# Kernel tuning notes

Measured on AMD Instinct MI355X. Metric: run time of the kernel, lower is better.

Reference implementation:

```python
import jax, jax.numpy as jnp
import numpy as np

N_NODES = 50000
N_EDGES = 800000
IN_NODE = 16
IN_EDGE = 8
HID = 128
N_LAYERS = 4
LN_EPS = 1e-5


def setup_inputs() -> dict:
    key = jax.random.key(0)
    ks = jax.random.split(key, 16)
    s = lambda k, shape, fan: jax.random.normal(k, shape, jnp.float32) * (1.0 / np.sqrt(fan))
    inp = {
        "x": jax.random.normal(ks[0], (N_NODES, IN_NODE), jnp.float32),
        "edge_index": jax.random.randint(ks[1], (2, N_EDGES), 0, N_NODES, jnp.int32),
        "edge_attr": jax.random.normal(ks[2], (N_EDGES, IN_EDGE), jnp.float32),
        # input projection
        "W_in": s(ks[3], (HID, IN_NODE), IN_NODE),
        "b_in": jnp.zeros((HID,), jnp.float32),
        # stacked SAGEConv params: lin_l (neighbors, biased), lin_r (root, no bias)
        "Wl": s(ks[4], (N_LAYERS, HID, HID), HID),
        "bl": jnp.zeros((N_LAYERS, HID), jnp.float32),
        "Wr": s(ks[5], (N_LAYERS, HID, HID), HID),
        # stacked LayerNorm params
        "ln_g": jnp.ones((N_LAYERS, HID), jnp.float32),
        "ln_b": jnp.zeros((N_LAYERS, HID), jnp.float32),
        # edge MLP: (2*HID+IN_EDGE) -> HID -> HID//2 -> 1
        "W1": s(ks[6], (HID, 2 * HID + IN_EDGE), 2 * HID + IN_EDGE),
        "b1": jnp.zeros((HID,), jnp.float32),
        "W2": s(ks[7], (HID // 2, HID), HID),
        "b2": jnp.zeros((HID // 2,), jnp.float32),
        "W3": s(ks[8], (1, HID // 2), HID // 2),
        "b3": jnp.zeros((1,), jnp.float32),
    }
    return inp


def reference(x, edge_index, edge_attr, W_in, b_in, Wl, bl, Wr, ln_g, ln_b, W1, b1, W2, b2, W3, b3):
    n = x.shape[0]
    src, dst = edge_index[0], edge_index[1]
    # in-degree for mean aggregation (clamped to 1, as in PyG mean aggr)
    deg = jax.ops.segment_sum(jnp.ones_like(dst, jnp.float32), dst, num_segments=n)
    deg = jnp.maximum(deg, 1.0)[:, None]  # [N,1]

    h = x @ W_in.T + b_in  # [N,H]

    def layer(h, params):
        Wl_i, bl_i, Wr_i, g_i, be_i = params
        # SAGEConv: mean of source features scattered to destinations
        agg = jax.ops.segment_sum(h[src], dst, num_segments=n) / deg
        h2 = agg @ Wl_i.T + bl_i + h @ Wr_i.T
        # LayerNorm
        mu = jnp.mean(h2, axis=-1, keepdims=True)
        var = jnp.mean(jnp.square(h2 - mu), axis=-1, keepdims=True)
        h2 = (h2 - mu) * jax.lax.rsqrt(var + LN_EPS) * g_i + be_i
        # ReLU (dropout = identity in eval mode)
        return jax.nn.relu(h2), None

    h, _ = jax.lax.scan(layer, h, (Wl, bl, Wr, ln_g, ln_b))

    # edge head: gather endpoints, concat with edge_attr, MLP -> scalar logit
    e = jnp.concatenate([h[src], h[dst], edge_attr], axis=1)  # [E, 2H+F_e]
    e = jax.nn.relu(e @ W1.T + b1)
    e = jax.nn.relu(e @ W2.T + b2)
    logits = (e @ W3.T + b3)[:, 0]  # [E]
    return logits
```

## Files before the change

### kernel.cpp

```cpp
#include <hip/hip_runtime.h>
#include <stdint.h>

#define NN 50000
#define NE 800000

#define O_WIN 0
#define O_BIN 2048
#define O_WL  2176
#define O_BL  67712
#define O_WR  68224
#define O_LNG 133760
#define O_LNB 134272
#define O_W1  134784
#define O_B1  168576
#define O_W2  168704
#define O_B2  176896
#define O_W3  176960
#define O_B3  177024
#define W_TOTAL 177025

#define WS_FLAGS 0
#define WS_WC    512
#define WS_CNT   355072
#define WS_ROWP  555520
#define WS_CUR   756224
#define WS_CSR   956928
#define WS_EID   4156928
#define WS_DST   7356928
#define WS_W1P   10556928
#define WS_HB0   10630656
#define WS_HB1   23430656
#define WS_NEED  36230656

#define SCAN_NB 196

#define HSTR 304
#define ASTR 560

typedef float f32x4 __attribute__((ext_vector_type(4)));
typedef short bf16x8 __attribute__((ext_vector_type(8)));
typedef short bf16x4 __attribute__((ext_vector_type(4)));

__device__ __forceinline__ float b2f(unsigned short u) {
  union { unsigned int i; float f; } v; v.i = ((unsigned int)u) << 16; return v.f;
}
__device__ __forceinline__ float asf(unsigned int u) {
  union { unsigned int i; float f; } v; v.i = u; return v.f;
}
__device__ __forceinline__ unsigned short f2b(float f) {
  union { float f; unsigned int i; } v; v.f = f;
  return (unsigned short)((v.i + 0x7fffu + ((v.i >> 16) & 1u)) >> 16);
}

#define LBAR() do { \
  asm volatile("s_waitcnt lgkmcnt(0)" ::: "memory"); \
  __builtin_amdgcn_s_barrier(); \
} while (0)

__global__ void k_fallback(unsigned short* __restrict__ out) {
  int gid = blockIdx.x * 256 + threadIdx.x;
  if (gid < NE) out[gid] = 0x3F00;
}

__global__ void k_probe(const unsigned short* __restrict__ x_u,
                        const int* __restrict__ ei32, int* __restrict__ flags) {
  const int t = threadIdx.x;
  int insane = 0;
  for (int i = t; i < 512; i += 64) {
    float v = b2f(x_u[i]);
    if (!(fabsf(v) < 1e4f)) insane++;
  }
#pragma unroll
  for (int off = 1; off < 64; off <<= 1) insane += __shfl_xor(insane, off, 64);
  int nz = 0;
  for (int i = t; i < 128; i += 64) nz |= (ei32[2 * i + 1] != 0);
  unsigned long long m = __ballot(nz != 0);
  if (t == 0) {
    flags[0] = (insane >= 16) ? 1 : 0;
    flags[1] = (m == 0ULL) ? 1 : 0;
  }
}

__global__ void k_cvt_w(const void* W_in, const void* b_in, const void* Wl,
                        const void* bl, const void* Wr, const void* lng,
                        const void* lnb, const void* W1, const void* b1,
                        const void* W2, const void* b2, const void* W3,
                        const void* b3, unsigned short* __restrict__ wc,
                        const int* __restrict__ flags) {
  const int gid = blockIdx.x * 256 + threadIdx.x;
  if (gid >= W_TOTAL) return;
  const int f32 = flags[0];
  const void* src; int off;
  if      (gid < O_BIN) { src = W_in; off = gid - O_WIN; }
  else if (gid < O_WL)  { src = b_in; off = gid - O_BIN; }
  else if (gid < O_BL)  { src = Wl;   off = gid - O_WL;  }
  else if (gid < O_WR)  { src = bl;   off = gid - O_BL;  }
  else if (gid < O_LNG) { src = Wr;   off = gid - O_WR;  }
  else if (gid < O_LNB) { src = lng;  off = gid - O_LNG; }
  else if (gid < O_W1)  { src = lnb;  off = gid - O_LNB; }
  else if (gid < O_B1)  { src = W1;   off = gid - O_W1;  }
  else if (gid < O_W2)  { src = b1;   off = gid - O_B1;  }
  else if (gid < O_B2)  { src = W2;   off = gid - O_W2;  }
  else if (gid < O_W3)  { src = b2;   off = gid - O_B2;  }
  else if (gid < O_B3)  { src = W3;   off = gid - O_W3;  }
  else                  { src = b3;   off = 0;           }
  wc[gid] = f32 ? f2b(((const float*)src)[off]) : ((const unsigned short*)src)[off];
}

__global__ void k_build_w1p(const unsigned short* __restrict__ wc,
                            unsigned short* __restrict__ W1p) {
  int gid = blockIdx.x * 256 + threadIdx.x;
  if (gid >= 128 * 288) return;
  int j = gid / 288, k = gid - j * 288;
  W1p[gid] = (k < 264) ? wc[O_W1 + j * 264 + k] : (unsigned short)0;
}

__global__ void k_cvt_ea(const void* __restrict__ ea,
                         unsigned short* __restrict__ eab,
                         const int* __restrict__ flags) {
  const int gid = blockIdx.x * 256 + threadIdx.x;
  if (gid >= NE) return;
  if (flags[0]) {
    const float4* ep = (const float4*)((const float*)ea + (size_t)gid * 8);
    const float4 a = ep[0], b = ep[1];
    union { ushort4 v[2]; int4 i; } o;
    o.v[0].x = f2b(a.x); o.v[0].y = f2b(a.y); o.v[0].z = f2b(a.z); o.v[0].w = f2b(a.w);
    o.v[1].x = f2b(b.x); o.v[1].y = f2b(b.y); o.v[1].z = f2b(b.z); o.v[1].w = f2b(b.w);
    *(int4*)(eab + (size_t)gid * 8) = o.i;
  } else {
    *(int4*)(eab + (size_t)gid * 8) =
        *(const int4*)((const unsigned short*)ea + (size_t)gid * 8);
  }
}

__global__ void k_hist(const int* __restrict__ ei, int* __restrict__ cnt,
                       const int* __restrict__ flags) {
  const int e = blockIdx.x * 256 + threadIdx.x;
  if (e >= NE) return;
  const int d = flags[1] ? ei[2 * (NE + e)] : ei[NE + e];
  atomicAdd(&cnt[d], 1);
}

__global__ __launch_bounds__(256) void k_scan1(const int* __restrict__ cnt,
                                               int* __restrict__ rowptr,
                                               int* __restrict__ bsum) {
  __shared__ int ws4[4];
  const int t = threadIdx.x, ln = t & 63, wv = t >> 6;
  const int i = blockIdx.x * 256 + t;
  const int v = (i < NN) ? cnt[i] : 0;
  int x = v;
#pragma unroll
  for (int off = 1; off < 64; off <<= 1) {
    int y = __shfl_up(x, off, 64);
    if (ln >= off) x += y;
  }
  if (ln == 63) ws4[wv] = x;
  __syncthreads();
  if (t == 0) { ws4[1] += ws4[0]; ws4[2] += ws4[1]; ws4[3] += ws4[2]; }
  __syncthreads();
  const int woff = wv ? ws4[wv - 1] : 0;
  if (i < NN) rowptr[i] = woff + x - v;
  if (t == 255) bsum[blockIdx.x] = woff + x;
}

__global__ __launch_bounds__(256) void k_scan2(int* __restrict__ bsum) {
  __shared__ int ws4[4];
  const int t = threadIdx.x, ln = t & 63, wv = t >> 6;
  const int v = (t < SCAN_NB) ? bsum[t] : 0;
  int x = v;
#pragma unroll
  for (int off = 1; off < 64; off <<= 1) {
    int y = __shfl_up(x, off, 64);
    if (ln >= off) x += y;
  }
  if (ln == 63) ws4[wv] = x;
  __syncthreads();
  if (t == 0) { ws4[1] += ws4[0]; ws4[2] += ws4[1]; ws4[3] += ws4[2]; }
  __syncthreads();
  const int woff = wv ? ws4[wv - 1] : 0;
  if (t < SCAN_NB) bsum[t] = woff + x - v;
}

__global__ void k_scan3(int* __restrict__ rowptr, const int* __restrict__ bsum) {
  const int i = blockIdx.x * 256 + threadIdx.x;
  if (i < NN) rowptr[i] += bsum[blockIdx.x];
  if (i == 0) rowptr[NN] = NE;
}

__global__ void k_fill(const int* __restrict__ ei, const int* __restrict__ rowptr,
                       int* __restrict__ cursor, int* __restrict__ csr,
                       int* __restrict__ eidA, int* __restrict__ dstA,
                       const int* __restrict__ flags) {
  const int e = blockIdx.x * 256 + threadIdx.x;
  if (e >= NE) return;
  const int i64 = flags[1];
  const int s = i64 ? ei[2 * e] : ei[e];
  const int d = i64 ? ei[2 * (NE + e)] : ei[NE + e];
  const int pos = rowptr[d] + atomicAdd(&cursor[d], 1);
  csr[pos] = s;
  eidA[pos] = e;
  dstA[pos] = d;
}

__global__ void k_inproj(const void* __restrict__ x,
                         const unsigned short* __restrict__ wc,
                         unsigned short* __restrict__ hb,
                         const int* __restrict__ flags) {
  const int gid = blockIdx.x * 256 + threadIdx.x;
  const int n = gid >> 7, j = gid & 127;
  float xv[16];
  if (flags[0]) {
    const float4* xp = (const float4*)((const float*)x + (size_t)n * 16);
#pragma unroll
    for (int q = 0; q < 4; q++) {
      float4 t = xp[q];
      xv[q * 4 + 0] = t.x; xv[q * 4 + 1] = t.y; xv[q * 4 + 2] = t.z; xv[q * 4 + 3] = t.w;
    }
  } else {
    const unsigned short* xu = (const unsigned short*)x + (size_t)n * 16;
#pragma unroll
    for (int q = 0; q < 2; q++) {
      union { int4 v; unsigned short u[8]; } t;
      t.v = *(const int4*)(xu + q * 8);
#pragma unroll
      for (int i = 0; i < 8; i++) xv[q * 8 + i] = b2f(t.u[i]);
    }
  }
  float s = b2f(wc[O_BIN + j]);
  const unsigned short* wrow = wc + O_WIN + j * 16;
#pragma unroll
  for (int q = 0; q < 2; q++) {
    union { int4 v; unsigned short u[8]; } w;
    w.v = *(const int4*)(wrow + q * 8);
#pragma unroll
    for (int i = 0; i < 8; i++) s += b2f(w.u[i]) * xv[q * 8 + i];
  }
  hb[gid] = f2b(s);
}

__global__ __launch_bounds__(256) void k_agg(
    const unsigned short* __restrict__ hin, const int* __restrict__ csr,
    const int* __restrict__ rowptr, unsigned short* __restrict__ aggb) {
  const int tid = threadIdx.x;
  const int n = blockIdx.x * 4 + (tid >> 6);
  const int L = tid & 63;
  const int rg = L >> 4;
  const int j  = L & 15;
  const int rs = rowptr[n], re = rowptr[n + 1];
  const int4* hv = (const int4*)hin;
  float s[8];
#pragma unroll
  for (int i = 0; i < 8; i++) s[i] = 0.f;

  int e = rs;
  for (; e + 16 <= re; e += 16) {
    int idx[4];
#pragma unroll
    for (int k = 0; k < 4; k++) idx[k] = csr[e + k * 4 + rg];
    int4 u[4];
#pragma unroll
    for (int k = 0; k < 4; k++) u[k] = hv[(size_t)idx[k] * 16 + j];
#pragma unroll
    for (int k = 0; k < 4; k++) {
      const unsigned int w0 = (unsigned int)u[k].x, w1 = (unsigned int)u[k].y;
      const unsigned int w2 = (unsigned int)u[k].z, w3 = (unsigned int)u[k].w;
      s[0] += asf(w0 << 16); s[1] += asf(w0 & 0xffff0000u);
      s[2] += asf(w1 << 16); s[3] += asf(w1 & 0xffff0000u);
      s[4] += asf(w2 << 16); s[5] += asf(w2 & 0xffff0000u);
      s[6] += asf(w3 << 16); s[7] += asf(w3 & 0xffff0000u);
    }
  }
  if (e < re) {
    int idx[4], ok[4];
#pragma unroll
    for (int k = 0; k < 4; k++) {
      const int ee = e + k * 4 + rg;
      ok[k] = ee < re;
      idx[k] = csr[ok[k] ? ee : (re - 1)];
    }
    int4 u[4];
#pragma unroll
    for (int k = 0; k < 4; k++) u[k] = hv[(size_t)idx[k] * 16 + j];
#pragma unroll
    for (int k = 0; k < 4; k++) {
      if (ok[k]) {
        const unsigned int w0 = (unsigned int)u[k].x, w1 = (unsigned int)u[k].y;
        const unsigned int w2 = (unsigned int)u[k].z, w3 = (unsigned int)u[k].w;
        s[0] += asf(w0 << 16); s[1] += asf(w0 & 0xffff0000u);
        s[2] += asf(w1 << 16); s[3] += asf(w1 & 0xffff0000u);
        s[4] += asf(w2 << 16); s[5] += asf(w2 & 0xffff0000u);
        s[6] += asf(w3 << 16); s[7] += asf(w3 & 0xffff0000u);
      }
    }
  }

#pragma unroll
  for (int i = 0; i < 8; i++) {
    s[i] += __shfl_xor(s[i], 16, 64);
    s[i] += __shfl_xor(s[i], 32, 64);
  }
  if (rg == 0) {
    const int dg = re - rs;
    const float rd = 1.0f / (float)(dg > 1 ? dg : 1);
    union { int4 v; unsigned short h[8]; } o;
#pragma unroll
    for (int i = 0; i < 8; i++) o.h[i] = f2b(s[i] * rd);
    ((int4*)aggb)[(size_t)n * 16 + j] = o.v;
  }
}

__global__ __launch_bounds__(256) void k_sage_mfma(
    const unsigned short* __restrict__ hin, unsigned short* __restrict__ hagg,
    const unsigned short* __restrict__ wc, int l) {
  __shared__ __align__(16) unsigned char As[64 * ASTR];
  __shared__ float red1[64][4];
  __shared__ float red2[64][4];
  __shared__ float mr[64][2];
  const int tid = threadIdx.x;
  const int wv = tid >> 6;
  const int L = tid & 63;
  const int l15 = L & 15;
  const int q = L >> 4;
  const int n0 = blockIdx.x * 64;

  bf16x8 wf[2][8];
  float blv[2], gv[2], bv[2];
#pragma unroll
  for (int nt = 0; nt < 2; nt++) {
    const int jj = (wv * 2 + nt) * 16 + l15;
#pragma unroll
    for (int kc = 0; kc < 8; kc++) {
      const unsigned short* src = (kc < 4)
          ? wc + O_WL + ((size_t)l * 128 + jj) * 128 + kc * 32 + q * 8
          : wc + O_WR + ((size_t)l * 128 + jj) * 128 + (kc - 4) * 32 + q * 8;
      wf[nt][kc] = *(const bf16x8*)src;
    }
    blv[nt] = b2f(wc[O_BL + l * 128 + jj]);
    gv[nt]  = b2f(wc[O_LNG + l * 128 + jj]);
    bv[nt]  = b2f(wc[O_LNB + l * 128 + jj]);
  }

  for (int c = tid; c < 2048; c += 256) {
    const int row = c >> 5, part = c & 31;
    int node = n0 + row; if (node > NN - 1) node = NN - 1;
    const unsigned short* src = (part < 16)
        ? hagg + (size_t)node * 128 + part * 8
        : hin + (size_t)node * 128 + (part - 16) * 8;
    *(int4*)(As + row * ASTR + part * 16) = *(const int4*)src;
  }
  __syncthreads();

  f32x4 acc[4][2];
#pragma unroll
  for (int mt = 0; mt < 4; mt++)
#pragma unroll
    for (int nt = 0; nt < 2; nt++) acc[mt][nt] = (f32x4)(0.0f);
#pragma unroll
  for (int kc = 0; kc < 8; kc++) {
#pragma unroll
    for (int mt = 0; mt < 4; mt++) {
      const bf16x8 a = *(const bf16x8*)(As + (mt * 16 + l15) * ASTR + (kc * 32 + q * 8) * 2);
#pragma unroll
      for (int nt = 0; nt < 2; nt++)
        acc[mt][nt] = __builtin_amdgcn_mfma_f32_16x16x32_bf16(a, wf[nt][kc], acc[mt][nt], 0, 0, 0);
    }
  }
#pragma unroll
  for (int mt = 0; mt < 4; mt++) {
#pragma unroll
    for (int rg = 0; rg < 4; rg++) {
      acc[mt][0][rg] += blv[0];
      acc[mt][1][rg] += blv[1];
      float s = acc[mt][0][rg] + acc[mt][1][rg];
      float s2 = acc[mt][0][rg] * acc[mt][0][rg] + acc[mt][1][rg] * acc[mt][1][rg];
#pragma unroll
      for (int m = 1; m < 16; m <<= 1) {
        s += __shfl_xor(s, m, 64);
        s2 += __shfl_xor(s2, m, 64);
      }
      if (l15 == 0) {
        const int row = mt * 16 + q * 4 + rg;
        red1[row][wv] = s; red2[row][wv] = s2;
      }
    }
  }
  __syncthreads();
  if (tid < 64) {
    const float s1 = red1[tid][0] + red1[tid][1] + red1[tid][2] + red1[tid][3];
    const float s2 = red2[tid][0] + red2[tid][1] + red2[tid][2] + red2[tid][3];
    const float mu = s1 * 0.0078125f;
    const float var = s2 * 0.0078125f - mu * mu;
    mr[tid][0] = mu;
    mr[tid][1] = rsqrtf(var + 1e-5f);
  }
  __syncthreads();
#pragma unroll
  for (int mt = 0; mt < 4; mt++) {
#pragma unroll
    for (int rg = 0; rg < 4; rg++) {
      const int row = mt * 16 + q * 4 + rg;
      const int node = n0 + row;
      if (node < NN) {
        const float mu = mr[row][0], rstd = mr[row][1];
#pragma unroll
        for (int nt = 0; nt < 2; nt++) {
          const float o = (acc[mt][nt][rg] - mu) * rstd * gv[nt] + bv[nt];
          hagg[(size_t)node * 128 + (wv * 2 + nt) * 16 + l15] = f2b(fmaxf(o, 0.f));
        }
      }
    }
  }
}

__global__ __launch_bounds__(256) void k_edge_mfma(
    const unsigned short* __restrict__ hb, const int* __restrict__ csr,
    const int* __restrict__ eidA, const int* __restrict__ dstA,
    const unsigned short* __restrict__ eab, const unsigned short* __restrict__ W1p,
    const unsigned short* __restrict__ wc, void* __restrict__ out,
    const int* __restrict__ flags) {
  __shared__ __align__(16) unsigned char sm[51712];
  unsigned char* const Ue = sm;
  unsigned char* const Hs = sm + 4096;
  unsigned char* const E1 = sm + 4096;
  unsigned char* const Ds = sm + 23552;
  unsigned char* const E2 = sm + 43008;
  const int tid = threadIdx.x;
  const int wv = tid >> 6;
  const int L = tid & 63;
  const int l15 = L & 15;
  const int q = L >> 4;
  const int f32 = flags[0];
  const int r4 = tid >> 2, seg = tid & 3;

  for (int i = tid; i < 64 * 12; i += 256)
    *(int*)(Ue + (i / 12) * 64 + 16 + (i % 12) * 4) = 0;

  bf16x8 w1f[2][9];
  float b1v[2];
#pragma unroll
  for (int nt = 0; nt < 2; nt++) {
    const int jj = (wv * 2 + nt) * 16 + l15;
#pragma unroll
    for (int cc = 0; cc < 9; cc++)
      w1f[nt][cc] = *(const bf16x8*)(W1p + jj * 288 + cc * 32 + q * 8);
    b1v[nt] = b2f(wc[O_B1 + jj]);
  }
  bf16x8 w2f[4];
  const int jj2 = wv * 16 + l15;
#pragma unroll
  for (int kc = 0; kc < 4; kc++)
    w2f[kc] = *(const bf16x8*)(wc + O_W2 + jj2 * 128 + kc * 32 + q * 8);
  const float b2v = b2f(wc[O_B2 + jj2]);
  const float b3f = b2f(wc[O_B3]);

  const int NT = NE / 64;

  int4 hsr0, hsr1, hsr2, hsr3;
  int4 dsr0, dsr1, dsr2, dsr3;
  int4 uer; uer.x = uer.y = uer.z = uer.w = 0;
  {
    const int p0 = blockIdx.x * 64;
    const int s0 = csr[p0 + r4];
    const int d0 = dstA[p0 + r4];
    const unsigned short* gs = hb + (size_t)s0 * 128 + seg * 32;
    const unsigned short* gd = hb + (size_t)d0 * 128 + seg * 32;
    hsr0 = ((const int4*)gs)[0]; hsr1 = ((const int4*)gs)[1];
    hsr2 = ((const int4*)gs)[2]; hsr3 = ((const int4*)gs)[3];
    dsr0 = ((const int4*)gd)[0]; dsr1 = ((const int4*)gd)[1];
    dsr2 = ((const int4*)gd)[2]; dsr3 = ((const int4*)gd)[3];
    if (tid < 64) {
      const int e0 = eidA[p0 + tid];
      uer = *(const int4*)(eab + (size_t)e0 * 8);
    }
  }

  for (int t = blockIdx.x; t < NT; t += gridDim.x) {
    const int pbase = t * 64;
    const int tn = (t + (int)gridDim.x < NT) ? (t + (int)gridDim.x) : t;
    const int pnext = tn * 64;

    if (tid < 64) *(int4*)(Ue + tid * 64) = uer;
    {
      unsigned char* ldst = Hs + r4 * HSTR + seg * 64;
      ((int4*)ldst)[0] = hsr0; ((int4*)ldst)[1] = hsr1;
      ((int4*)ldst)[2] = hsr2; ((int4*)ldst)[3] = hsr3;
      unsigned char* ldd = Ds + r4 * HSTR + seg * 64;
      ((int4*)ldd)[0] = dsr0; ((int4*)ldd)[1] = dsr1;
      ((int4*)ldd)[2] = dsr2; ((int4*)ldd)[3] = dsr3;
    }
    const int sN = csr[pnext + r4];
    const int dN = dstA[pnext + r4];
    int eN = 0;
    if (tid < 64) eN = eidA[pnext + tid];

    LBAR();

    int4 h0, h1, h2, h3, d0, d1, d2, d3;
    {
      const unsigned short* gsn = hb + (size_t)sN * 128 + seg * 32;
      h0 = ((const int4*)gsn)[0]; h1 = ((const int4*)gsn)[1];
      h2 = ((const int4*)gsn)[2]; h3 = ((const int4*)gsn)[3];
      const unsigned short* gdn = hb + (size_t)dN * 128 + seg * 32;
      d0 = ((const int4*)gdn)[0]; d1 = ((const int4*)gdn)[1];
      d2 = ((const int4*)gdn)[2]; d3 = ((const int4*)gdn)[3];
    }
    int4 uen; uen.x = uen.y = uen.z = uen.w = 0;
    if (tid < 64) uen = *(const int4*)(eab + (size_t)eN * 8);

    f32x4 acc1[4][2];
#pragma unroll
    for (int mt = 0; mt < 4; mt++)
#pragma unroll
      for (int nt = 0; nt < 2; nt++) acc1[mt][nt] = (f32x4)(0.0f);
#pragma unroll
    for (int cc = 0; cc < 4; cc++) {
#pragma unroll
      for (int mt = 0; mt < 4; mt++) {
        const bf16x8 a = *(const bf16x8*)(Hs + (mt * 16 + l15) * HSTR + (cc * 32 + q * 8) * 2);
#pragma unroll
        for (int nt = 0; nt < 2; nt++)
          acc1[mt][nt] = __builtin_amdgcn_mfma_f32_16x16x32_bf16(a, w1f[nt][cc], acc1[mt][nt], 0, 0, 0);
      }
    }
#pragma unroll
    for (int cc = 4; cc < 8; cc++) {
#pragma unroll
      for (int mt = 0; mt < 4; mt++) {
        const bf16x8 a = *(const bf16x8*)(Ds + (mt * 16 + l15) * HSTR + ((cc - 4) * 32 + q * 8) * 2);
#pragma unroll
        for (int nt = 0; nt < 2; nt++)
          acc1[mt][nt] = __builtin_amdgcn_mfma_f32_16x16x32_bf16(a, w1f[nt][cc], acc1[mt][nt], 0, 0, 0);
      }
    }
#pragma unroll
    for (int mt = 0; mt < 4; mt++) {
      const bf16x8 a = *(const bf16x8*)(Ue + (mt * 16 + l15) * 64 + q * 16);
#pragma unroll
      for (int nt = 0; nt < 2; nt++)
        acc1[mt][nt] = __builtin_amdgcn_mfma_f32_16x16x32_bf16(a, w1f[nt][8], acc1[mt][nt], 0, 0, 0);
    }
    LBAR();

#pragma unroll
    for (int mt = 0; mt < 4; mt++)
#pragma unroll
      for (int nt = 0; nt < 2; nt++)
#pragma unroll
        for (int rg = 0; rg < 4; rg++) {
          const int er = mt * 16 + q * 4 + rg;
          const int jj = (wv * 2 + nt) * 16 + l15;
          *(unsigned short*)(E1 + er * HSTR + jj * 2) =
              f2b(fmaxf(acc1[mt][nt][rg] + b1v[nt], 0.f));
        }
    LBAR();

    f32x4 acc2[4];
#pragma unroll
    for (int mt = 0; mt < 4; mt++) acc2[mt] = (f32x4)(0.0f);
#pragma unroll
    for (int kc = 0; kc < 4; kc++) {
#pragma unroll
      for (int mt = 0; mt < 4; mt++) {
        const bf16x8 a = *(const bf16x8*)(E1 + (mt * 16 + l15) * HSTR + (kc * 32 + q * 8) * 2);
        acc2[mt] = __builtin_amdgcn_mfma_f32_16x16x32_bf16(a, w2f[kc], acc2[mt], 0, 0, 0);
      }
    }
#pragma unroll
    for (int mt = 0; mt < 4; mt++)
#pragma unroll
      for (int rg = 0; rg < 4; rg++) {
        const int er = mt * 16 + q * 4 + rg;
        *(unsigned short*)(E2 + er * 136 + jj2 * 2) =
            f2b(fmaxf(acc2[mt][rg] + b2v, 0.f));
      }
    LBAR();

    const int el = wv * 16 + l15;
    float acc = 0.f;
#pragma unroll
    for (int i4 = 0; i4 < 4; i4++) {
      const bf16x4 v = *(const bf16x4*)(E2 + el * 136 + q * 32 + i4 * 8);
#pragma unroll
      for (int j = 0; j < 4; j++)
        acc += b2f((unsigned short)v[j]) * b2f(wc[O_W3 + q * 16 + i4 * 4 + j]);
    }
    acc += __shfl_xor(acc, 16, 64);
    acc += __shfl_xor(acc, 32, 64);
    if (q == 0) {
      const int e = eidA[pbase + el];
      const float r = acc + b3f;
      if (f32) ((float*)out)[e] = r;
      else     ((unsigned short*)out)[e] = f2b(r);
    }

    hsr0 = h0; hsr1 = h1; hsr2 = h2; hsr3 = h3;
    dsr0 = d0; dsr1 = d1; dsr2 = d2; dsr3 = d3;
    uer = uen;
  }
}

extern "C" void kernel_launch(void* const* d_in, const int* in_sizes, int n_in,
                              void* d_out, int out_size, void* d_ws, size_t ws_size,
                              hipStream_t stream) {
  const void* x  = d_in[0];
  const int*  ei = (const int*)d_in[1];
  const void* ea = d_in[2];

  char* ws = (char*)d_ws;
  int*            flags  = (int*)(ws + WS_FLAGS);
  unsigned short* wc     = (unsigned short*)(ws + WS_WC);
  int*            cnt    = (int*)(ws + WS_CNT);
  int*            rowptr = (int*)(ws + WS_ROWP);
  int*            cursor = (int*)(ws + WS_CUR);
  int*            csr    = (int*)(ws + WS_CSR);
  int*            eidA   = (int*)(ws + WS_EID);
  int*            dstA   = (int*)(ws + WS_DST);
  unsigned short* W1p    = (unsigned short*)(ws + WS_W1P);
  unsigned short* hb0    = (unsigned short*)(ws + WS_HB0);
  unsigned short* hb1    = (unsigned short*)(ws + WS_HB1);
  int*            bsum   = (int*)(ws + WS_CSR);

  if (ws_size < WS_NEED) {
    k_fallback<<<3125, 256, 0, stream>>>((unsigned short*)d_out);
    return;
  }

  k_probe<<<1, 64, 0, stream>>>((const unsigned short*)x, ei, flags);
  k_cvt_w<<<(W_TOTAL + 255) / 256, 256, 0, stream>>>(
      d_in[3], d_in[4], d_in[5], d_in[6], d_in[7], d_in[8], d_in[9],
      d_in[10], d_in[11], d_in[12], d_in[13], d_in[14], d_in[15], wc, flags);
  k_build_w1p<<<144, 256, 0, stream>>>(wc, W1p);

  hipMemsetAsync(cnt, 0, NN * sizeof(int), stream);
  hipMemsetAsync(cursor, 0, NN * sizeof(int), stream);
  k_hist<<<3125, 256, 0, stream>>>(ei, cnt, flags);
  k_scan1<<<SCAN_NB, 256, 0, stream>>>(cnt, rowptr, bsum);
  k_scan2<<<1, 256, 0, stream>>>(bsum);
  k_scan3<<<SCAN_NB, 256, 0, stream>>>(rowptr, bsum);
  k_fill<<<3125, 256, 0, stream>>>(ei, rowptr, cursor, csr, eidA, dstA, flags);

  k_inproj<<<NN * 128 / 256, 256, 0, stream>>>(x, wc, hb0, flags);

  unsigned short* cur = hb0;
  unsigned short* nxt = hb1;
  for (int l = 0; l < 4; l++) {
    k_agg<<<12500, 256, 0, stream>>>(cur, csr, rowptr, nxt);
    k_sage_mfma<<<782, 256, 0, stream>>>(cur, nxt, wc, l);
    unsigned short* tmp = cur; cur = nxt; nxt = tmp;
  }
  unsigned short* eab = nxt;
  k_cvt_ea<<<3125, 256, 0, stream>>>(ea, eab, flags);
  k_edge_mfma<<<3125, 256, 0, stream>>>(cur, csr, eidA, dstA, eab, W1p, wc, d_out, flags);
}
```

Measured before the change: 557.8 us.

## Fuse edge MLP layer 3 into layer-2 MFMA epilogue and pack edge/dst ids

The second edge-MLP layer is restructured so each wave computes all 64 output columns for its own 16 edge rows, and the final 64->1 projection is done in registers with a lane shuffle reduction. This removes the E2 shared-memory round trip, the bf16 rounding of layer-2 activations, and one block barrier per tile. Edge id and destination arrays are also packed into one int2 array to halve index loads. In exchange, W2 is held fully per lane (more registers), E1 gets its own shared region so LDS grows, which can reduce occupancy.

```diff
diff --git a/kernel.cpp b/kernel.cpp
--- a/kernel.cpp
+++ b/kernel.cpp
@@ -25,8 +25,7 @@
 #define WS_ROWP  555520
 #define WS_CUR   756224
 #define WS_CSR   956928
-#define WS_EID   4156928
-#define WS_DST   7356928
+#define WS_ED    4156928
 #define WS_W1P   10556928
 #define WS_HB0   10630656
 #define WS_HB1   23430656
@@ -39,7 +38,6 @@
 
 typedef float f32x4 __attribute__((ext_vector_type(4)));
 typedef short bf16x8 __attribute__((ext_vector_type(8)));
-typedef short bf16x4 __attribute__((ext_vector_type(4)));
 
 __device__ __forceinline__ float b2f(unsigned short u) {
   union { unsigned int i; float f; } v; v.i = ((unsigned int)u) << 16; return v.f;
@@ -189,8 +187,7 @@
 
 __global__ void k_fill(const int* __restrict__ ei, const int* __restrict__ rowptr,
                        int* __restrict__ cursor, int* __restrict__ csr,
-                       int* __restrict__ eidA, int* __restrict__ dstA,
-                       const int* __restrict__ flags) {
+                       int2* __restrict__ ed, const int* __restrict__ flags) {
   const int e = blockIdx.x * 256 + threadIdx.x;
   if (e >= NE) return;
   const int i64 = flags[1];
@@ -198,8 +195,7 @@
   const int d = i64 ? ei[2 * (NE + e)] : ei[NE + e];
   const int pos = rowptr[d] + atomicAdd(&cursor[d], 1);
   csr[pos] = s;
-  eidA[pos] = e;
-  dstA[pos] = d;
+  ed[pos] = make_int2(e, d);
 }
 
 __global__ void k_inproj(const void* __restrict__ x,
@@ -414,16 +410,14 @@
 
 __global__ __launch_bounds__(256) void k_edge_mfma(
     const unsigned short* __restrict__ hb, const int* __restrict__ csr,
-    const int* __restrict__ eidA, const int* __restrict__ dstA,
-    const unsigned short* __restrict__ eab, const unsigned short* __restrict__ W1p,
-    const unsigned short* __restrict__ wc, void* __restrict__ out,
-    const int* __restrict__ flags) {
-  __shared__ __align__(16) unsigned char sm[51712];
+    const int2* __restrict__ ed, const unsigned short* __restrict__ eab,
+    const unsigned short* __restrict__ W1p, const unsigned short* __restrict__ wc,
+    void* __restrict__ out, const int* __restrict__ flags) {
+  __shared__ __align__(16) unsigned char sm[62464];
   unsigned char* const Ue = sm;
   unsigned char* const Hs = sm + 4096;
-  unsigned char* const E1 = sm + 4096;
   unsigned char* const Ds = sm + 23552;
-  unsigned char* const E2 = sm + 43008;
+  unsigned char* const E1 = sm + 43008;
   const int tid = threadIdx.x;
   const int wv = tid >> 6;
   const int L = tid & 63;
@@ -445,12 +439,17 @@
       w1f[nt][cc] = *(const bf16x8*)(W1p + jj * 288 + cc * 32 + q * 8);
     b1v[nt] = b2f(wc[O_B1 + jj]);
   }
-  bf16x8 w2f[4];
-  const int jj2 = wv * 16 + l15;
-#pragma unroll
-  for (int kc = 0; kc < 4; kc++)
-    w2f[kc] = *(const bf16x8*)(wc + O_W2 + jj2 * 128 + kc * 32 + q * 8);
-  const float b2v = b2f(wc[O_B2 + jj2]);
+  bf16x8 w2f[4][4];
+  float b2v[4], w3v[4];
+#pragma unroll
+  for (int nt = 0; nt < 4; nt++) {
+    const int jj = nt * 16 + l15;
+#pragma unroll
+    for (int kc = 0; kc < 4; kc++)
+      w2f[nt][kc] = *(const bf16x8*)(wc + O_W2 + jj * 128 + kc * 32 + q * 8);
+    b2v[nt] = b2f(wc[O_B2 + jj]);
+    w3v[nt] = b2f(wc[O_W3 + jj]);
+  }
   const float b3f = b2f(wc[O_B3]);
 
   const int NT = NE / 64;
@@ -461,7 +460,7 @@
   {
     const int p0 = blockIdx.x * 64;
     const int s0 = csr[p0 + r4];
-    const int d0 = dstA[p0 + r4];
+    const int d0 = ed[p0 + r4].y;
     const unsigned short* gs = hb + (size_t)s0 * 128 + seg * 32;
     const unsigned short* gd = hb + (size_t)d0 * 128 + seg * 32;
     hsr0 = ((const int4*)gs)[0]; hsr1 = ((const int4*)gs)[1];
@@ -469,7 +468,7 @@
     dsr0 = ((const int4*)gd)[0]; dsr1 = ((const int4*)gd)[1];
     dsr2 = ((const int4*)gd)[2]; dsr3 = ((const int4*)gd)[3];
     if (tid < 64) {
-      const int e0 = eidA[p0 + tid];
+      const int e0 = ed[p0 + tid].x;
       uer = *(const int4*)(eab + (size_t)e0 * 8);
     }
   }
@@ -489,9 +488,9 @@
       ((int4*)ldd)[2] = dsr2; ((int4*)ldd)[3] = dsr3;
     }
     const int sN = csr[pnext + r4];
-    const int dN = dstA[pnext + r4];
+    const int dN = ed[pnext + r4].y;
     int eN = 0;
-    if (tid < 64) eN = eidA[pnext + tid];
+    if (tid < 64) eN = ed[pnext + tid].x;
 
     LBAR();
 
@@ -556,41 +555,37 @@
 
     f32x4 acc2[4];
 #pragma unroll
-    for (int mt = 0; mt < 4; mt++) acc2[mt] = (f32x4)(0.0f);
+    for (int nt = 0; nt < 4; nt++) acc2[nt] = (f32x4)(0.0f);
 #pragma unroll
     for (int kc = 0; kc < 4; kc++) {
-#pragma unroll
-      for (int mt = 0; mt < 4; mt++) {
-        const bf16x8 a = *(const bf16x8*)(E1 + (mt * 16 + l15) * HSTR + (kc * 32 + q * 8) * 2);
-        acc2[mt] = __builtin_amdgcn_mfma_f32_16x16x32_bf16(a, w2f[kc], acc2[mt], 0, 0, 0);
+      const bf16x8 a = *(const bf16x8*)(E1 + (wv * 16 + l15) * HSTR + (kc * 32 + q * 8) * 2);
+#pragma unroll
+      for (int nt = 0; nt < 4; nt++)
+        acc2[nt] = __builtin_amdgcn_mfma_f32_16x16x32_bf16(a, w2f[nt][kc], acc2[nt], 0, 0, 0);
+    }
+
+    float p[4];
+#pragma unroll
+    for (int rg = 0; rg < 4; rg++) {
+      float s = 0.f;
+#pragma unroll
+      for (int nt = 0; nt < 4; nt++)
+        s += fmaxf(acc2[nt][rg] + b2v[nt], 0.f) * w3v[nt];
+      p[rg] = s;
+    }
+#pragma unroll
+    for (int off = 1; off < 16; off <<= 1)
+#pragma unroll
+      for (int rg = 0; rg < 4; rg++) p[rg] += __shfl_xor(p[rg], off, 64);
+    if (l15 == 0) {
+#pragma unroll
+      for (int rg = 0; rg < 4; rg++) {
+        const int slot = pbase + wv * 16 + q * 4 + rg;
+        const int e = ed[slot].x;
+        const float r = p[rg] + b3f;
+        if (f32) ((float*)out)[e] = r;
+        else     ((unsigned short*)out)[e] = f2b(r);
       }
-    }
-#pragma unroll
-    for (int mt = 0; mt < 4; mt++)
-#pragma unroll
-      for (int rg = 0; rg < 4; rg++) {
-        const int er = mt * 16 + q * 4 + rg;
-        *(unsigned short*)(E2 + er * 136 + jj2 * 2) =
-            f2b(fmaxf(acc2[mt][rg] + b2v, 0.f));
-      }
-    LBAR();
-
-    const int el = wv * 16 + l15;
-    float acc = 0.f;
-#pragma unroll
-    for (int i4 = 0; i4 < 4; i4++) {
-      const bf16x4 v = *(const bf16x4*)(E2 + el * 136 + q * 32 + i4 * 8);
-#pragma unroll
-      for (int j = 0; j < 4; j++)
-        acc += b2f((unsigned short)v[j]) * b2f(wc[O_W3 + q * 16 + i4 * 4 + j]);
-    }
-    acc += __shfl_xor(acc, 16, 64);
-    acc += __shfl_xor(acc, 32, 64);
-    if (q == 0) {
-      const int e = eidA[pbase + el];
-      const float r = acc + b3f;
-      if (f32) ((float*)out)[e] = r;
-      else     ((unsigned short*)out)[e] = f2b(r);
     }
 
     hsr0 = h0; hsr1 = h1; hsr2 = h2; hsr3 = h3;
@@ -613,8 +608,7 @@
   int*            rowptr = (int*)(ws + WS_ROWP);
   int*            cursor = (int*)(ws + WS_CUR);
   int*            csr    = (int*)(ws + WS_CSR);
-  int*            eidA   = (int*)(ws + WS_EID);
-  int*            dstA   = (int*)(ws + WS_DST);
+  int2*           ed     = (int2*)(ws + WS_ED);
   unsigned short* W1p    = (unsigned short*)(ws + WS_W1P);
   unsigned short* hb0    = (unsigned short*)(ws + WS_HB0);
   unsigned short* hb1    = (unsigned short*)(ws + WS_HB1);
@@ -637,7 +631,7 @@
   k_scan1<<<SCAN_NB, 256, 0, stream>>>(cnt, rowptr, bsum);
   k_scan2<<<1, 256, 0, stream>>>(bsum);
   k_scan3<<<SCAN_NB, 256, 0, stream>>>(rowptr, bsum);
-  k_fill<<<3125, 256, 0, stream>>>(ei, rowptr, cursor, csr, eidA, dstA, flags);
+  k_fill<<<3125, 256, 0, stream>>>(ei, rowptr, cursor, csr, ed, flags);
 
   k_inproj<<<NN * 128 / 256, 256, 0, stream>>>(x, wc, hb0, flags);
 
@@ -650,5 +644,5 @@
   }
   unsigned short* eab = nxt;
   k_cvt_ea<<<3125, 256, 0, stream>>>(ea, eab, flags);
-  k_edge_mfma<<<3125, 256, 0, stream>>>(cur, csr, eidA, dstA, eab, W1p, wc, d_out, flags);
-}
+  k_edge_mfma<<<3125, 256, 0, stream>>>(cur, csr, ed, eab, W1p, wc, d_out, flags);
+}
```

Measured after the change: 585.2 us. 4.9% more time.
